# Kernel optimization log

Measured on AMD Instinct MI355X. Metric: run time of the kernel, lower is better.

## Reference

```python
import jax, jax.numpy as jnp
import numpy as np

NUM_HEADS = 4
NUM_GROUPS = 8
EPS = 1e-5


def setup_inputs() -> dict:
    key = jax.random.key(0)
    ks = jax.random.split(key, 4)
    B, C, H, W = 4, 256, 64, 64
    x = jax.random.normal(ks[0], (B, C, H, W), dtype=jnp.float32)
    gn_w = jnp.ones((C,), dtype=jnp.float32)
    gn_b = jnp.zeros((C,), dtype=jnp.float32)
    # 1x1 convs == per-pixel matmuls; store kernels as [out_ch, in_ch]
    w_qkv = jax.random.normal(ks[1], (3 * C, C), dtype=jnp.float32) * (1.0 / np.sqrt(C))
    b_qkv = jnp.zeros((3 * C,), dtype=jnp.float32)
    w_proj = jax.random.normal(ks[2], (C, C), dtype=jnp.float32) * (1.0 / np.sqrt(C))
    b_proj = jnp.zeros((C,), dtype=jnp.float32)
    return {"x": x, "gn_w": gn_w, "gn_b": gn_b, "w_qkv": w_qkv,
            "b_qkv": b_qkv, "w_proj": w_proj, "b_proj": b_proj}


def reference(x, gn_w, gn_b, w_qkv, b_qkv, w_proj, b_proj):
    B, C, H, W = x.shape
    N = H * W
    nh = NUM_HEADS
    dh = C // nh

    # GroupNorm(8, C)
    xg = x.reshape(B, NUM_GROUPS, C // NUM_GROUPS, N)
    mu = jnp.mean(xg, axis=(2, 3), keepdims=True)
    var = jnp.var(xg, axis=(2, 3), keepdims=True)
    h = ((xg - mu) * jax.lax.rsqrt(var + EPS)).reshape(B, C, N)
    h = h * gn_w[None, :, None] + gn_b[None, :, None]

    # qkv 1x1 conv
    qkv = jnp.einsum('oc,bcn->bon', w_qkv, h) + b_qkv[None, :, None]
    q, k, v = jnp.split(qkv, 3, axis=1)  # each [B, C, N]
    q = q.reshape(B, nh, dh, N)
    k = k.reshape(B, nh, dh, N)
    v = v.reshape(B, nh, dh, N)

    # attn = softmax(q^T k / sqrt(dh)) over last dim -> [B, nh, N, N]
    scores = jnp.einsum('bhdi,bhdj->bhij', q, k) / jnp.sqrt(jnp.array(dh, dtype=x.dtype))
    attn = jax.nn.softmax(scores, axis=-1)

    # out = attn @ v^T, back to channel-major layout
    out = jnp.einsum('bhij,bhdj->bhdi', attn, v).reshape(B, C, N)

    # proj_out 1x1 conv + residual
    out = jnp.einsum('oc,bcn->bon', w_proj, out) + b_proj[None, :, None]
    return x + out.reshape(B, C, H, W)
```

## Files before the change

### kernel.cpp

```cpp
#include <hip/hip_runtime.h>
#include <math.h>

#define N_PIX 4096
#define C_CH  256
#define NH    4
#define DH    64

typedef __attribute__((ext_vector_type(8))) short bf16x8;
typedef __attribute__((ext_vector_type(4))) float f32x4;

static __device__ __forceinline__ unsigned short f2bf(float f) {
  union { float f; unsigned u; } v; v.f = f;
  unsigned r = v.u + 0x7fffu + ((v.u >> 16) & 1u);
  return (unsigned short)(r >> 16);
}
static __device__ __forceinline__ unsigned pk2(float a, float b) {
  return (unsigned)f2bf(a) | ((unsigned)f2bf(b) << 16);
}
static __device__ __forceinline__ unsigned pk2t(float a, float b) {
  return __builtin_amdgcn_perm(__float_as_uint(b), __float_as_uint(a),
                               0x07060302u);
}
#if __has_builtin(__builtin_amdgcn_exp2f)
#define EXP2(x) __builtin_amdgcn_exp2f(x)
#else
#define EXP2(x) exp2f(x)
#endif
static __device__ __forceinline__ int swz(int row, int g) {
  return (row << 6) + ((((row >> 2) ^ row ^ g) & 7) << 3);
}

__global__ __launch_bounds__(256) void gn_part_kernel(
    const float* __restrict__ x, float* __restrict__ part) {
  const int g = blockIdx.x, b = blockIdx.y, z = blockIdx.z;
  const float* base = x + (size_t)(b * C_CH + g * 32 + z * 4) * N_PIX;
  const int t = threadIdx.x;
  float sum = 0.f, sq = 0.f;
  for (int i = t * 4; i < 4 * N_PIX; i += 256 * 4) {
    float4 v = *(const float4*)(base + i);
    sum += v.x + v.y + v.z + v.w;
    sq  += v.x * v.x + v.y * v.y + v.z * v.z + v.w * v.w;
  }
  for (int off = 32; off >= 1; off >>= 1) {
    sum += __shfl_down(sum, off, 64);
    sq  += __shfl_down(sq,  off, 64);
  }
  __shared__ float ps[4], pq[4];
  if ((t & 63) == 0) { ps[t >> 6] = sum; pq[t >> 6] = sq; }
  __syncthreads();
  if (t == 0) {
    int idx = ((b * 8 + g) * 8 + z) * 2;
    part[idx + 0] = ps[0] + ps[1] + ps[2] + ps[3];
    part[idx + 1] = pq[0] + pq[1] + pq[2] + pq[3];
  }
}

__global__ __launch_bounds__(64) void gn_finish_kernel(
    const float* __restrict__ part, const float* __restrict__ gn_w,
    const float* __restrict__ gn_b, float* __restrict__ scale,
    float* __restrict__ shift) {
  const int g = blockIdx.x, b = blockIdx.y, t = threadIdx.x;
  if (t >= 32) return;
  float S = 0.f, Q = 0.f;
#pragma unroll
  for (int z = 0; z < 8; ++z) {
    int idx = ((b * 8 + g) * 8 + z) * 2;
    S += part[idx + 0];
    Q += part[idx + 1];
  }
  const float inv_cnt = 1.f / (32.f * N_PIX);
  float mu  = S * inv_cnt;
  float var = Q * inv_cnt - mu * mu;
  float rstd = rsqrtf(var + 1e-5f);
  int c = g * 32 + t;
  float s = rstd * gn_w[c];
  scale[b * C_CH + c] = s;
  shift[b * C_CH + c] = gn_b[c] - mu * s;
}

__global__ __launch_bounds__(256) void wcvt_kernel(
    const float* __restrict__ wqkv, const float* __restrict__ wproj,
    unsigned short* __restrict__ wB) {
  const int i = blockIdx.x * 256 + threadIdx.x;
  const float* src = (i < 49152) ? (wqkv + (size_t)i * 4)
                                 : (wproj + (size_t)(i - 49152) * 4);
  float4 v = *(const float4*)src;
  uint2 u;
  u.x = pk2(v.x, v.y);
  u.y = pk2(v.z, v.w);
  *(uint2*)(wB + (size_t)i * 4) = u;
}

__global__ __launch_bounds__(256) void gn_apply_kernel(
    const float* __restrict__ x, const float* __restrict__ scale,
    const float* __restrict__ shift, unsigned short* __restrict__ hT) {
  const int n0 = blockIdx.x * 64;
  const int c0 = blockIdx.y * 64;
  const int b  = blockIdx.z;
  const int t  = threadIdx.x;
  __shared__ unsigned short Ht[64 * 64];
  const int cl = t >> 4;
  const int nl = (t & 15) * 4;
#pragma unroll
  for (int r = 0; r < 4; ++r) {
    int c = c0 + cl + r * 16;
    float sv = scale[b * C_CH + c], sh = shift[b * C_CH + c];
    float4 v = *(const float4*)(x + ((size_t)(b * C_CH + c)) * N_PIX + n0 + nl);
    int ce = cl + r * 16;
#pragma unroll
    for (int i = 0; i < 4; ++i) {
      float f = ((const float*)&v)[i] * sv + sh;
      Ht[swz(nl + i, ce >> 3) + (ce & 7)] = f2bf(f);
    }
  }
  __syncthreads();
  {
    const int row = t >> 2, sg = (t & 3) * 2;
    uint4 o0 = *(const uint4*)&Ht[swz(row, sg + 0)];
    uint4 o1 = *(const uint4*)&Ht[swz(row, sg + 1)];
    size_t go = ((size_t)(b * N_PIX + n0 + row)) * C_CH + c0 + sg * 8;
    *(uint4*)(hT + go) = o0;
    *(uint4*)(hT + go + 8) = o1;
  }
}

__global__ __launch_bounds__(256) void qkv_gemm_kernel(
    const unsigned short* __restrict__ hT, const unsigned short* __restrict__ wB,
    const float* __restrict__ bqkv, unsigned short* __restrict__ qT,
    unsigned short* __restrict__ kT, unsigned short* __restrict__ vO) {
  const int mb = blockIdx.x, type = mb >> 2, head = mb & 3;
  const int n0 = blockIdx.y * 128;
  const int b  = blockIdx.z;
  const int t  = threadIdx.x;
  const int wave = t >> 6, lane = t & 63, quad = lane >> 4, lc = lane & 15;

  __shared__ unsigned short Ws[64 * 64];
  __shared__ unsigned short Hs[128 * 64];

  f32x4 acc[4][2];
#pragma unroll
  for (int i = 0; i < 4; ++i)
#pragma unroll
    for (int j = 0; j < 2; ++j) acc[i][j] = (f32x4){0.f, 0.f, 0.f, 0.f};

  const int wrow = t >> 2, wgb = (t & 3) * 2;
  const int hrow = t >> 1, hgb = (t & 1) * 4;
  const unsigned short* wp = wB + (size_t)(mb * 64 + wrow) * C_CH;
  const unsigned short* ap =
      hT + ((size_t)(b * N_PIX + n0 + hrow)) * C_CH + hgb * 8;

  for (int k0 = 0; k0 < C_CH; k0 += 64) {
    __syncthreads();
    {
      const unsigned short* s0 = wp + k0 + wgb * 8;
      uint4 u0 = *(const uint4*)(s0);
      uint4 u1 = *(const uint4*)(s0 + 8);
      *(uint4*)&Ws[swz(wrow, wgb + 0)] = u0;
      *(uint4*)&Ws[swz(wrow, wgb + 1)] = u1;
    }
    {
      const unsigned short* s0 = ap + k0;
#pragma unroll
      for (int j = 0; j < 4; ++j) {
        uint4 u = *(const uint4*)(s0 + j * 8);
        *(uint4*)&Hs[swz(hrow, hgb + j)] = u;
      }
    }
    __syncthreads();
#pragma unroll
    for (int kh = 0; kh < 2; ++kh) {
      bf16x8 wf[4], hf[2];
#pragma unroll
      for (int mt = 0; mt < 4; ++mt)
        wf[mt] = *(const bf16x8*)&Ws[swz(mt * 16 + lc, kh * 4 + quad)];
#pragma unroll
      for (int nt = 0; nt < 2; ++nt)
        hf[nt] = *(const bf16x8*)&Hs[swz(wave * 32 + nt * 16 + lc, kh * 4 + quad)];
      if (type < 2) {
#pragma unroll
        for (int mt = 0; mt < 4; ++mt)
#pragma unroll
          for (int nt = 0; nt < 2; ++nt)
            acc[mt][nt] = __builtin_amdgcn_mfma_f32_16x16x32_bf16(
                wf[mt], hf[nt], acc[mt][nt], 0, 0, 0);
      } else {
#pragma unroll
        for (int mt = 0; mt < 4; ++mt)
#pragma unroll
          for (int nt = 0; nt < 2; ++nt)
            acc[mt][nt] = __builtin_amdgcn_mfma_f32_16x16x32_bf16(
                hf[nt], wf[mt], acc[mt][nt], 0, 0, 0);
      }
    }
  }

  if (type < 2) {
    unsigned short* dst = (type == 0) ? qT : kT;
    const float qs = (type == 0) ? 0.125f * 1.44269504f : 1.0f;
#pragma unroll
    for (int mt = 0; mt < 4; ++mt)
#pragma unroll
      for (int nt = 0; nt < 2; ++nt) {
        int n = n0 + wave * 32 + nt * 16 + lc;
        int d0 = mt * 16 + quad * 4;
        float b0 = bqkv[mb * 64 + d0 + 0], b1 = bqkv[mb * 64 + d0 + 1];
        float b2 = bqkv[mb * 64 + d0 + 2], b3 = bqkv[mb * 64 + d0 + 3];
        uint2 w;
        w.x = pk2((acc[mt][nt][0] + b0) * qs, (acc[mt][nt][1] + b1) * qs);
        w.y = pk2((acc[mt][nt][2] + b2) * qs, (acc[mt][nt][3] + b3) * qs);
        *(uint2*)(dst + ((size_t)((b * NH + head) * N_PIX + n)) * 64 + d0) = w;
      }
  } else {
#pragma unroll
    for (int mt = 0; mt < 4; ++mt)
#pragma unroll
      for (int nt = 0; nt < 2; ++nt) {
        int d = mt * 16 + lc;
        float bias = bqkv[mb * 64 + d];
        int pix = n0 + wave * 32 + nt * 16 + quad * 4;
        uint2 w;
        w.x = pk2(acc[mt][nt][0] + bias, acc[mt][nt][1] + bias);
        w.y = pk2(acc[mt][nt][2] + bias, acc[mt][nt][3] + bias);
        *(uint2*)(vO + ((size_t)((b * NH + head) * 64 + d)) * N_PIX + pix) = w;
      }
  }
}

__global__ __launch_bounds__(256) void attn_kernel(
    const unsigned short* __restrict__ qT, const unsigned short* __restrict__ kT,
    const unsigned short* __restrict__ vO, unsigned short* __restrict__ aT) {
  const int t  = threadIdx.x;
  const int i0 = blockIdx.x * 64;
  const int h  = blockIdx.y;
  const int b  = blockIdx.z;
  const size_t bh = (size_t)(b * NH + h);
  const unsigned short* qp = qT + bh * N_PIX * 64;
  const unsigned short* kp = kT + bh * N_PIX * 64;
  const unsigned short* vp = vO + bh * 64 * N_PIX;

  __shared__ unsigned short Qt[64 * 64];
  __shared__ unsigned short Kt[64 * 64];
  __shared__ unsigned short Vs[64 * 64];
  __shared__ unsigned short Ps[64 * 64];

  const int wave = t >> 6, lane = t & 63, quad = lane >> 4, lc = lane & 15;
  const int qbase = wave * 16;
  const int srow = t >> 2, sg = (t & 3) * 2;

  {
    const unsigned short* s = qp + (size_t)(i0 + srow) * 64 + sg * 8;
    uint4 a0 = *(const uint4*)(s);
    uint4 a1 = *(const uint4*)(s + 8);
    *(uint4*)&Qt[swz(srow, sg + 0)] = a0;
    *(uint4*)&Qt[swz(srow, sg + 1)] = a1;
  }
  __syncthreads();
  const bf16x8 aq0 = *(const bf16x8*)&Qt[swz(qbase + lc, quad)];
  const bf16x8 aq1 = *(const bf16x8*)&Qt[swz(qbase + lc, quad + 4)];

  int kof0[4], kof1[4], pw[4], vof0[4], vof1[4];
#pragma unroll
  for (int jt = 0; jt < 4; ++jt) {
    kof0[jt] = swz(jt * 16 + lc, quad);
    kof1[jt] = swz(jt * 16 + lc, quad + 4);
    pw[jt]   = swz(qbase + lc, jt * 2 + (quad >> 1)) + (quad & 1) * 4;
  }
#pragma unroll
  for (int mt = 0; mt < 4; ++mt) {
    vof0[mt] = swz(mt * 16 + lc, quad);
    vof1[mt] = swz(mt * 16 + lc, quad + 4);
  }
  const int pb0 = swz(qbase + lc, quad), pb1 = swz(qbase + lc, quad + 4);
  const bf16x8 ones = {16256, 16256, 16256, 16256, 16256, 16256, 16256, 16256};

  f32x4 la = (f32x4){0.f, 0.f, 0.f, 0.f};
  f32x4 od[4];
#pragma unroll
  for (int mt = 0; mt < 4; ++mt) od[mt] = (f32x4){0.f, 0.f, 0.f, 0.f};

  for (int j0 = 0; j0 < N_PIX; j0 += 64) {
    __syncthreads();
    {
      const unsigned short* sk = kp + (size_t)(j0 + srow) * 64 + sg * 8;
      uint4 k0 = *(const uint4*)(sk);
      uint4 k1 = *(const uint4*)(sk + 8);
      *(uint4*)&Kt[swz(srow, sg + 0)] = k0;
      *(uint4*)&Kt[swz(srow, sg + 1)] = k1;
      const unsigned short* sv = vp + (size_t)srow * N_PIX + j0 + sg * 8;
      uint4 v0 = *(const uint4*)(sv);
      uint4 v1 = *(const uint4*)(sv + 8);
      *(uint4*)&Vs[swz(srow, sg + 0)] = v0;
      *(uint4*)&Vs[swz(srow, sg + 1)] = v1;
    }
    __syncthreads();

#pragma unroll
    for (int jt = 0; jt < 4; ++jt) {
      bf16x8 bk0 = *(const bf16x8*)&Kt[kof0[jt]];
      bf16x8 bk1 = *(const bf16x8*)&Kt[kof1[jt]];
      f32x4 a = (f32x4){0.f, 0.f, 0.f, 0.f};
      a = __builtin_amdgcn_mfma_f32_16x16x32_bf16(bk0, aq0, a, 0, 0, 0);
      a = __builtin_amdgcn_mfma_f32_16x16x32_bf16(bk1, aq1, a, 0, 0, 0);
      uint2 u;
      u.x = pk2t(EXP2(a[0]), EXP2(a[1]));
      u.y = pk2t(EXP2(a[2]), EXP2(a[3]));
      *(uint2*)&Ps[pw[jt]] = u;
    }

    bf16x8 bp0 = *(const bf16x8*)&Ps[pb0];
    bf16x8 bp1 = *(const bf16x8*)&Ps[pb1];
    la = __builtin_amdgcn_mfma_f32_16x16x32_bf16(ones, bp0, la, 0, 0, 0);
    la = __builtin_amdgcn_mfma_f32_16x16x32_bf16(ones, bp1, la, 0, 0, 0);
#pragma unroll
    for (int mt = 0; mt < 4; ++mt) {
      bf16x8 av0 = *(const bf16x8*)&Vs[vof0[mt]];
      bf16x8 av1 = *(const bf16x8*)&Vs[vof1[mt]];
      od[mt] = __builtin_amdgcn_mfma_f32_16x16x32_bf16(av0, bp0, od[mt], 0, 0, 0);
      od[mt] = __builtin_amdgcn_mfma_f32_16x16x32_bf16(av1, bp1, od[mt], 0, 0, 0);
    }
  }

  __syncthreads();
  float inv = 1.f / la[0];
#pragma unroll
  for (int mt = 0; mt < 4; ++mt) {
    uint2 u;
    u.x = pk2(od[mt][0] * inv, od[mt][1] * inv);
    u.y = pk2(od[mt][2] * inv, od[mt][3] * inv);
    *(uint2*)&Ps[swz(qbase + lc, mt * 2 + (quad >> 1)) + (quad & 1) * 4] = u;
  }
  __syncthreads();
  {
    uint4 o0 = *(const uint4*)&Ps[swz(srow, sg + 0)];
    uint4 o1 = *(const uint4*)&Ps[swz(srow, sg + 1)];
    size_t go = ((size_t)(b * N_PIX + i0 + srow)) * C_CH + h * 64 + sg * 8;
    *(uint4*)(aT + go) = o0;
    *(uint4*)(aT + go + 8) = o1;
  }
}

__global__ __launch_bounds__(256) void proj_gemm_kernel(
    const unsigned short* __restrict__ aT, const unsigned short* __restrict__ wPB,
    const float* __restrict__ bproj, const float* __restrict__ x,
    float* __restrict__ out) {
  const int m0 = blockIdx.x * 64;
  const int n0 = blockIdx.y * 128;
  const int b  = blockIdx.z;
  const int t  = threadIdx.x;
  const int wave = t >> 6, lane = t & 63, quad = lane >> 4, lc = lane & 15;

  __shared__ unsigned short Ws[64 * 64];
  __shared__ unsigned short Hs[128 * 64];

  f32x4 acc[4][2];
#pragma unroll
  for (int i = 0; i < 4; ++i)
#pragma unroll
    for (int j = 0; j < 2; ++j) acc[i][j] = (f32x4){0.f, 0.f, 0.f, 0.f};

  const int wrow = t >> 2, wgb = (t & 3) * 2;
  const int hrow = t >> 1, hgb = (t & 1) * 4;
  const unsigned short* wp = wPB + (size_t)(m0 + wrow) * C_CH;
  const unsigned short* ap =
      aT + ((size_t)(b * N_PIX + n0 + hrow)) * C_CH + hgb * 8;

  for (int k0 = 0; k0 < C_CH; k0 += 64) {
    __syncthreads();
    {
      const unsigned short* s0 = wp + k0 + wgb * 8;
      uint4 u0 = *(const uint4*)(s0);
      uint4 u1 = *(const uint4*)(s0 + 8);
      *(uint4*)&Ws[swz(wrow, wgb + 0)] = u0;
      *(uint4*)&Ws[swz(wrow, wgb + 1)] = u1;
    }
    {
      const unsigned short* s0 = ap + k0;
#pragma unroll
      for (int j = 0; j < 4; ++j) {
        uint4 u = *(const uint4*)(s0 + j * 8);
        *(uint4*)&Hs[swz(hrow, hgb + j)] = u;
      }
    }
    __syncthreads();
#pragma unroll
    for (int kh = 0; kh < 2; ++kh) {
      bf16x8 wf[4], hf[2];
#pragma unroll
      for (int mt = 0; mt < 4; ++mt)
        wf[mt] = *(const bf16x8*)&Ws[swz(mt * 16 + lc, kh * 4 + quad)];
#pragma unroll
      for (int nt = 0; nt < 2; ++nt)
        hf[nt] = *(const bf16x8*)&Hs[swz(wave * 32 + nt * 16 + lc, kh * 4 + quad)];
#pragma unroll
      for (int mt = 0; mt < 4; ++mt)
#pragma unroll
        for (int nt = 0; nt < 2; ++nt)
          acc[mt][nt] = __builtin_amdgcn_mfma_f32_16x16x32_bf16(
              wf[mt], hf[nt], acc[mt][nt], 0, 0, 0);
    }
  }
#pragma unroll
  for (int mt = 0; mt < 4; ++mt) {
#pragma unroll
    for (int nt = 0; nt < 2; ++nt) {
      int n = n0 + wave * 32 + nt * 16 + lc;
#pragma unroll
      for (int r = 0; r < 4; ++r) {
        int c = m0 + mt * 16 + quad * 4 + r;
        size_t gi = ((size_t)(b * C_CH + c)) * N_PIX + n;
        out[gi] = acc[mt][nt][r] + bproj[c] + x[gi];
      }
    }
  }
}

extern "C" void kernel_launch(void* const* d_in, const int* in_sizes, int n_in,
                              void* d_out, int out_size, void* d_ws,
                              size_t ws_size, hipStream_t stream) {
  const float* x      = (const float*)d_in[0];
  const float* gn_w   = (const float*)d_in[1];
  const float* gn_b   = (const float*)d_in[2];
  const float* w_qkv  = (const float*)d_in[3];
  const float* b_qkv  = (const float*)d_in[4];
  const float* w_proj = (const float*)d_in[5];
  const float* b_proj = (const float*)d_in[6];
  float* out = (float*)d_out;

  float* ws    = (float*)d_ws;
  float* scale = ws;
  float* shift = ws + 1024;
  float* part  = ws + 2048;
  unsigned short* qT = (unsigned short*)(ws + 4096);
  unsigned short* kT = qT + (size_t)4194304;
  unsigned short* vO = kT + (size_t)4194304;
  unsigned short* aT = vO + (size_t)4194304;
  unsigned short* hT = aT + (size_t)4194304;
  unsigned short* wB = hT + (size_t)4 * N_PIX * C_CH;
  unsigned short* wPB = wB + (size_t)49152 * 4;

  gn_part_kernel<<<dim3(8, 4, 8), dim3(256), 0, stream>>>(x, part);
  gn_finish_kernel<<<dim3(8, 4), dim3(64), 0, stream>>>(part, gn_w, gn_b,
                                                        scale, shift);
  wcvt_kernel<<<dim3(256), dim3(256), 0, stream>>>(w_qkv, w_proj, wB);
  gn_apply_kernel<<<dim3(64, 4, 4), dim3(256), 0, stream>>>(x, scale, shift,
                                                            hT);
  qkv_gemm_kernel<<<dim3(12, 32, 4), dim3(256), 0, stream>>>(
      hT, wB, b_qkv, qT, kT, vO);
  attn_kernel<<<dim3(64, 4, 4), dim3(256), 0, stream>>>(qT, kT, vO, aT);
  proj_gemm_kernel<<<dim3(4, 32, 4), dim3(256), 0, stream>>>(
      aT, wPB, b_proj, x, out);
}
```

Before: 225.6 us.

## Double attention query tile per block and fuse small GroupNorm/weight-convert kernels

The attention kernel now processes 128 query rows per block, 32 per wave as two 16-row sub-tiles. Each K/V tile staged in LDS is reused for twice as many queries, halving global K/V traffic and the number of blocks. The P scratch buffer is aliased onto the Q LDS buffer to keep shared memory usage similar. Separately, weight bf16 conversion is folded into gn_part and the GroupNorm finish step into gn_apply, removing two launches. The trade-off is fewer blocks (512) and more accumulator registers per wave, which may lower occupancy.

```diff
diff --git a/kernel.cpp b/kernel.cpp
--- a/kernel.cpp
+++ b/kernel.cpp
@@ -31,10 +31,23 @@
 }
 
 __global__ __launch_bounds__(256) void gn_part_kernel(
-    const float* __restrict__ x, float* __restrict__ part) {
+    const float* __restrict__ x, const float* __restrict__ wqkv,
+    const float* __restrict__ wproj, float* __restrict__ part,
+    unsigned short* __restrict__ wB) {
   const int g = blockIdx.x, b = blockIdx.y, z = blockIdx.z;
+  const int t = threadIdx.x;
+  {
+    const int bid = blockIdx.z * 32 + blockIdx.y * 8 + blockIdx.x;
+    const int i = bid * 256 + t;
+    const float* src = (i < 49152) ? (wqkv + (size_t)i * 4)
+                                   : (wproj + (size_t)(i - 49152) * 4);
+    float4 v = *(const float4*)src;
+    uint2 u;
+    u.x = pk2(v.x, v.y);
+    u.y = pk2(v.z, v.w);
+    *(uint2*)(wB + (size_t)i * 4) = u;
+  }
   const float* base = x + (size_t)(b * C_CH + g * 32 + z * 4) * N_PIX;
-  const int t = threadIdx.x;
   float sum = 0.f, sq = 0.f;
   for (int i = t * 4; i < 4 * N_PIX; i += 256 * 4) {
     float4 v = *(const float4*)(base + i);
@@ -55,58 +68,43 @@
   }
 }
 
-__global__ __launch_bounds__(64) void gn_finish_kernel(
-    const float* __restrict__ part, const float* __restrict__ gn_w,
-    const float* __restrict__ gn_b, float* __restrict__ scale,
-    float* __restrict__ shift) {
-  const int g = blockIdx.x, b = blockIdx.y, t = threadIdx.x;
-  if (t >= 32) return;
-  float S = 0.f, Q = 0.f;
-#pragma unroll
-  for (int z = 0; z < 8; ++z) {
-    int idx = ((b * 8 + g) * 8 + z) * 2;
-    S += part[idx + 0];
-    Q += part[idx + 1];
-  }
-  const float inv_cnt = 1.f / (32.f * N_PIX);
-  float mu  = S * inv_cnt;
-  float var = Q * inv_cnt - mu * mu;
-  float rstd = rsqrtf(var + 1e-5f);
-  int c = g * 32 + t;
-  float s = rstd * gn_w[c];
-  scale[b * C_CH + c] = s;
-  shift[b * C_CH + c] = gn_b[c] - mu * s;
-}
-
-__global__ __launch_bounds__(256) void wcvt_kernel(
-    const float* __restrict__ wqkv, const float* __restrict__ wproj,
-    unsigned short* __restrict__ wB) {
-  const int i = blockIdx.x * 256 + threadIdx.x;
-  const float* src = (i < 49152) ? (wqkv + (size_t)i * 4)
-                                 : (wproj + (size_t)(i - 49152) * 4);
-  float4 v = *(const float4*)src;
-  uint2 u;
-  u.x = pk2(v.x, v.y);
-  u.y = pk2(v.z, v.w);
-  *(uint2*)(wB + (size_t)i * 4) = u;
-}
-
 __global__ __launch_bounds__(256) void gn_apply_kernel(
-    const float* __restrict__ x, const float* __restrict__ scale,
-    const float* __restrict__ shift, unsigned short* __restrict__ hT) {
+    const float* __restrict__ x, const float* __restrict__ part,
+    const float* __restrict__ gn_w, const float* __restrict__ gn_b,
+    unsigned short* __restrict__ hT) {
   const int n0 = blockIdx.x * 64;
   const int c0 = blockIdx.y * 64;
   const int b  = blockIdx.z;
   const int t  = threadIdx.x;
   __shared__ unsigned short Ht[64 * 64];
+  __shared__ float ls[64], lsh[64];
+  if (t < 64) {
+    int c = c0 + t;
+    int g = c >> 5;
+    float S = 0.f, Q = 0.f;
+#pragma unroll
+    for (int z = 0; z < 8; ++z) {
+      int idx = ((b * 8 + g) * 8 + z) * 2;
+      S += part[idx + 0];
+      Q += part[idx + 1];
+    }
+    const float inv_cnt = 1.f / (32.f * N_PIX);
+    float mu  = S * inv_cnt;
+    float var = Q * inv_cnt - mu * mu;
+    float rstd = rsqrtf(var + 1e-5f);
+    float s = rstd * gn_w[c];
+    ls[t]  = s;
+    lsh[t] = gn_b[c] - mu * s;
+  }
+  __syncthreads();
   const int cl = t >> 4;
   const int nl = (t & 15) * 4;
 #pragma unroll
   for (int r = 0; r < 4; ++r) {
-    int c = c0 + cl + r * 16;
-    float sv = scale[b * C_CH + c], sh = shift[b * C_CH + c];
-    float4 v = *(const float4*)(x + ((size_t)(b * C_CH + c)) * N_PIX + n0 + nl);
     int ce = cl + r * 16;
+    float sv = ls[ce], sh = lsh[ce];
+    float4 v =
+        *(const float4*)(x + ((size_t)(b * C_CH + c0 + ce)) * N_PIX + n0 + nl);
 #pragma unroll
     for (int i = 0; i < 4; ++i) {
       float f = ((const float*)&v)[i] * sv + sh;
@@ -230,7 +228,7 @@
     const unsigned short* __restrict__ qT, const unsigned short* __restrict__ kT,
     const unsigned short* __restrict__ vO, unsigned short* __restrict__ aT) {
   const int t  = threadIdx.x;
-  const int i0 = blockIdx.x * 64;
+  const int i0 = blockIdx.x * 128;
   const int h  = blockIdx.y;
   const int b  = blockIdx.z;
   const size_t bh = (size_t)(b * NH + h);
@@ -238,45 +236,55 @@
   const unsigned short* kp = kT + bh * N_PIX * 64;
   const unsigned short* vp = vO + bh * 64 * N_PIX;
 
-  __shared__ unsigned short Qt[64 * 64];
+  __shared__ unsigned short Qt[128 * 64];
   __shared__ unsigned short Kt[64 * 64];
   __shared__ unsigned short Vs[64 * 64];
-  __shared__ unsigned short Ps[64 * 64];
+  unsigned short* const Ps = Qt;
 
   const int wave = t >> 6, lane = t & 63, quad = lane >> 4, lc = lane & 15;
-  const int qbase = wave * 16;
+  const int qb0 = wave * 32, qb1 = wave * 32 + 16;
   const int srow = t >> 2, sg = (t & 3) * 2;
+  const int qrow = t >> 1, qg = (t & 1) * 4;
 
   {
-    const unsigned short* s = qp + (size_t)(i0 + srow) * 64 + sg * 8;
-    uint4 a0 = *(const uint4*)(s);
-    uint4 a1 = *(const uint4*)(s + 8);
-    *(uint4*)&Qt[swz(srow, sg + 0)] = a0;
-    *(uint4*)&Qt[swz(srow, sg + 1)] = a1;
+    const unsigned short* s = qp + (size_t)(i0 + qrow) * 64 + qg * 8;
+#pragma unroll
+    for (int i = 0; i < 4; ++i) {
+      uint4 u = *(const uint4*)(s + i * 8);
+      *(uint4*)&Qt[swz(qrow, qg + i)] = u;
+    }
   }
   __syncthreads();
-  const bf16x8 aq0 = *(const bf16x8*)&Qt[swz(qbase + lc, quad)];
-  const bf16x8 aq1 = *(const bf16x8*)&Qt[swz(qbase + lc, quad + 4)];
-
-  int kof0[4], kof1[4], pw[4], vof0[4], vof1[4];
+  bf16x8 aq[2][2];
+  aq[0][0] = *(const bf16x8*)&Qt[swz(qb0 + lc, quad)];
+  aq[0][1] = *(const bf16x8*)&Qt[swz(qb0 + lc, quad + 4)];
+  aq[1][0] = *(const bf16x8*)&Qt[swz(qb1 + lc, quad)];
+  aq[1][1] = *(const bf16x8*)&Qt[swz(qb1 + lc, quad + 4)];
+
+  int kof0[4], kof1[4], vof0[4], vof1[4], pw[2][4];
 #pragma unroll
   for (int jt = 0; jt < 4; ++jt) {
     kof0[jt] = swz(jt * 16 + lc, quad);
     kof1[jt] = swz(jt * 16 + lc, quad + 4);
-    pw[jt]   = swz(qbase + lc, jt * 2 + (quad >> 1)) + (quad & 1) * 4;
+    pw[0][jt] = swz(qb0 + lc, jt * 2 + (quad >> 1)) + (quad & 1) * 4;
+    pw[1][jt] = swz(qb1 + lc, jt * 2 + (quad >> 1)) + (quad & 1) * 4;
   }
 #pragma unroll
   for (int mt = 0; mt < 4; ++mt) {
     vof0[mt] = swz(mt * 16 + lc, quad);
     vof1[mt] = swz(mt * 16 + lc, quad + 4);
   }
-  const int pb0 = swz(qbase + lc, quad), pb1 = swz(qbase + lc, quad + 4);
+  const int pb00 = swz(qb0 + lc, quad), pb01 = swz(qb0 + lc, quad + 4);
+  const int pb10 = swz(qb1 + lc, quad), pb11 = swz(qb1 + lc, quad + 4);
   const bf16x8 ones = {16256, 16256, 16256, 16256, 16256, 16256, 16256, 16256};
 
-  f32x4 la = (f32x4){0.f, 0.f, 0.f, 0.f};
-  f32x4 od[4];
-#pragma unroll
-  for (int mt = 0; mt < 4; ++mt) od[mt] = (f32x4){0.f, 0.f, 0.f, 0.f};
+  f32x4 la0 = (f32x4){0.f, 0.f, 0.f, 0.f};
+  f32x4 la1 = (f32x4){0.f, 0.f, 0.f, 0.f};
+  f32x4 od[2][4];
+#pragma unroll
+  for (int qh = 0; qh < 2; ++qh)
+#pragma unroll
+    for (int mt = 0; mt < 4; ++mt) od[qh][mt] = (f32x4){0.f, 0.f, 0.f, 0.f};
 
   for (int j0 = 0; j0 < N_PIX; j0 += 64) {
     __syncthreads();
@@ -298,44 +306,65 @@
     for (int jt = 0; jt < 4; ++jt) {
       bf16x8 bk0 = *(const bf16x8*)&Kt[kof0[jt]];
       bf16x8 bk1 = *(const bf16x8*)&Kt[kof1[jt]];
-      f32x4 a = (f32x4){0.f, 0.f, 0.f, 0.f};
-      a = __builtin_amdgcn_mfma_f32_16x16x32_bf16(bk0, aq0, a, 0, 0, 0);
-      a = __builtin_amdgcn_mfma_f32_16x16x32_bf16(bk1, aq1, a, 0, 0, 0);
-      uint2 u;
-      u.x = pk2t(EXP2(a[0]), EXP2(a[1]));
-      u.y = pk2t(EXP2(a[2]), EXP2(a[3]));
-      *(uint2*)&Ps[pw[jt]] = u;
-    }
-
-    bf16x8 bp0 = *(const bf16x8*)&Ps[pb0];
-    bf16x8 bp1 = *(const bf16x8*)&Ps[pb1];
-    la = __builtin_amdgcn_mfma_f32_16x16x32_bf16(ones, bp0, la, 0, 0, 0);
-    la = __builtin_amdgcn_mfma_f32_16x16x32_bf16(ones, bp1, la, 0, 0, 0);
+      f32x4 a0 = (f32x4){0.f, 0.f, 0.f, 0.f};
+      a0 = __builtin_amdgcn_mfma_f32_16x16x32_bf16(bk0, aq[0][0], a0, 0, 0, 0);
+      a0 = __builtin_amdgcn_mfma_f32_16x16x32_bf16(bk1, aq[0][1], a0, 0, 0, 0);
+      f32x4 a1 = (f32x4){0.f, 0.f, 0.f, 0.f};
+      a1 = __builtin_amdgcn_mfma_f32_16x16x32_bf16(bk0, aq[1][0], a1, 0, 0, 0);
+      a1 = __builtin_amdgcn_mfma_f32_16x16x32_bf16(bk1, aq[1][1], a1, 0, 0, 0);
+      uint2 u0, u1;
+      u0.x = pk2t(EXP2(a0[0]), EXP2(a0[1]));
+      u0.y = pk2t(EXP2(a0[2]), EXP2(a0[3]));
+      u1.x = pk2t(EXP2(a1[0]), EXP2(a1[1]));
+      u1.y = pk2t(EXP2(a1[2]), EXP2(a1[3]));
+      *(uint2*)&Ps[pw[0][jt]] = u0;
+      *(uint2*)&Ps[pw[1][jt]] = u1;
+    }
+
+    bf16x8 bp00 = *(const bf16x8*)&Ps[pb00];
+    bf16x8 bp01 = *(const bf16x8*)&Ps[pb01];
+    bf16x8 bp10 = *(const bf16x8*)&Ps[pb10];
+    bf16x8 bp11 = *(const bf16x8*)&Ps[pb11];
+    la0 = __builtin_amdgcn_mfma_f32_16x16x32_bf16(ones, bp00, la0, 0, 0, 0);
+    la0 = __builtin_amdgcn_mfma_f32_16x16x32_bf16(ones, bp01, la0, 0, 0, 0);
+    la1 = __builtin_amdgcn_mfma_f32_16x16x32_bf16(ones, bp10, la1, 0, 0, 0);
+    la1 = __builtin_amdgcn_mfma_f32_16x16x32_bf16(ones, bp11, la1, 0, 0, 0);
+
 #pragma unroll
     for (int mt = 0; mt < 4; ++mt) {
       bf16x8 av0 = *(const bf16x8*)&Vs[vof0[mt]];
       bf16x8 av1 = *(const bf16x8*)&Vs[vof1[mt]];
-      od[mt] = __builtin_amdgcn_mfma_f32_16x16x32_bf16(av0, bp0, od[mt], 0, 0, 0);
-      od[mt] = __builtin_amdgcn_mfma_f32_16x16x32_bf16(av1, bp1, od[mt], 0, 0, 0);
-    }
-  }
-
-  __syncthreads();
-  float inv = 1.f / la[0];
+      od[0][mt] =
+          __builtin_amdgcn_mfma_f32_16x16x32_bf16(av0, bp00, od[0][mt], 0, 0, 0);
+      od[0][mt] =
+          __builtin_amdgcn_mfma_f32_16x16x32_bf16(av1, bp01, od[0][mt], 0, 0, 0);
+      od[1][mt] =
+          __builtin_amdgcn_mfma_f32_16x16x32_bf16(av0, bp10, od[1][mt], 0, 0, 0);
+      od[1][mt] =
+          __builtin_amdgcn_mfma_f32_16x16x32_bf16(av1, bp11, od[1][mt], 0, 0, 0);
+    }
+  }
+
+  float inv0 = 1.f / la0[0];
+  float inv1 = 1.f / la1[0];
 #pragma unroll
   for (int mt = 0; mt < 4; ++mt) {
-    uint2 u;
-    u.x = pk2(od[mt][0] * inv, od[mt][1] * inv);
-    u.y = pk2(od[mt][2] * inv, od[mt][3] * inv);
-    *(uint2*)&Ps[swz(qbase + lc, mt * 2 + (quad >> 1)) + (quad & 1) * 4] = u;
+    uint2 u0, u1;
+    u0.x = pk2(od[0][mt][0] * inv0, od[0][mt][1] * inv0);
+    u0.y = pk2(od[0][mt][2] * inv0, od[0][mt][3] * inv0);
+    u1.x = pk2(od[1][mt][0] * inv1, od[1][mt][1] * inv1);
+    u1.y = pk2(od[1][mt][2] * inv1, od[1][mt][3] * inv1);
+    *(uint2*)&Ps[swz(qb0 + lc, mt * 2 + (quad >> 1)) + (quad & 1) * 4] = u0;
+    *(uint2*)&Ps[swz(qb1 + lc, mt * 2 + (quad >> 1)) + (quad & 1) * 4] = u1;
   }
   __syncthreads();
   {
-    uint4 o0 = *(const uint4*)&Ps[swz(srow, sg + 0)];
-    uint4 o1 = *(const uint4*)&Ps[swz(srow, sg + 1)];
-    size_t go = ((size_t)(b * N_PIX + i0 + srow)) * C_CH + h * 64 + sg * 8;
-    *(uint4*)(aT + go) = o0;
-    *(uint4*)(aT + go + 8) = o1;
+    size_t go = ((size_t)(b * N_PIX + i0 + qrow)) * C_CH + h * 64 + qg * 8;
+#pragma unroll
+    for (int i = 0; i < 4; ++i) {
+      uint4 o = *(const uint4*)&Ps[swz(qrow, qg + i)];
+      *(uint4*)(aT + go + i * 8) = o;
+    }
   }
 }
 
@@ -426,10 +455,8 @@
   const float* b_proj = (const float*)d_in[6];
   float* out = (float*)d_out;
 
-  float* ws    = (float*)d_ws;
-  float* scale = ws;
-  float* shift = ws + 1024;
-  float* part  = ws + 2048;
+  float* ws   = (float*)d_ws;
+  float* part = ws + 2048;
   unsigned short* qT = (unsigned short*)(ws + 4096);
   unsigned short* kT = qT + (size_t)4194304;
   unsigned short* vO = kT + (size_t)4194304;
@@ -438,15 +465,13 @@
   unsigned short* wB = hT + (size_t)4 * N_PIX * C_CH;
   unsigned short* wPB = wB + (size_t)49152 * 4;
 
-  gn_part_kernel<<<dim3(8, 4, 8), dim3(256), 0, stream>>>(x, part);
-  gn_finish_kernel<<<dim3(8, 4), dim3(64), 0, stream>>>(part, gn_w, gn_b,
-                                                        scale, shift);
-  wcvt_kernel<<<dim3(256), dim3(256), 0, stream>>>(w_qkv, w_proj, wB);
-  gn_apply_kernel<<<dim3(64, 4, 4), dim3(256), 0, stream>>>(x, scale, shift,
-                                                            hT);
+  gn_part_kernel<<<dim3(8, 4, 8), dim3(256), 0, stream>>>(x, w_qkv, w_proj,
+                                                          part, wB);
+  gn_apply_kernel<<<dim3(64, 4, 4), dim3(256), 0, stream>>>(x, part, gn_w,
+                                                            gn_b, hT);
   qkv_gemm_kernel<<<dim3(12, 32, 4), dim3(256), 0, stream>>>(
       hT, wB, b_qkv, qT, kT, vO);
-  attn_kernel<<<dim3(64, 4, 4), dim3(256), 0, stream>>>(qT, kT, vO, aT);
+  attn_kernel<<<dim3(32, 4, 4), dim3(256), 0, stream>>>(qT, kT, vO, aT);
   proj_gemm_kernel<<<dim3(4, 32, 4), dim3(256), 0, stream>>>(
       aT, wPB, b_proj, x, out);
 }
```

Result: no change. 223.2 us (-1.1%).
